# Optimization experiments

Measured on AMD Instinct MI355X. Metric: run time of the kernel, lower is better.

The kernel has to match this reference:

```python
import jax, jax.numpy as jnp
import numpy as np

B, N, D, H = 2, 2048, 1024, 16
DH = D // H
SCALE = DH ** -0.5


def setup_inputs() -> dict:
    key = jax.random.key(0)
    ks = jax.random.split(key, 12)
    s = 0.02
    q = jax.random.normal(ks[0], (B, N, D), jnp.float32)
    k = jax.random.normal(ks[1], (B, N, D), jnp.float32)
    v = jax.random.normal(ks[2], (B, N, D), jnp.float32)
    attn_mask = jax.random.randint(ks[3], (B, 1, N, N), 0, 2).astype(bool)
    Wq = jax.random.normal(ks[4], (D, D), jnp.float32) * s
    bq = jnp.zeros((D,), jnp.float32)
    Wk = jax.random.normal(ks[5], (D, D), jnp.float32) * s
    bk = jnp.zeros((D,), jnp.float32)
    Wv = jax.random.normal(ks[6], (D, D), jnp.float32) * s
    bv = jnp.zeros((D,), jnp.float32)
    Wp = jax.random.normal(ks[7], (D, D), jnp.float32) * s
    bp = jnp.zeros((D,), jnp.float32)
    return {"q": q, "k": k, "v": v, "attn_mask": attn_mask,
            "Wq": Wq, "bq": bq, "Wk": Wk, "bk": bk,
            "Wv": Wv, "bv": bv, "Wp": Wp, "bp": bp}


def _heads(x, W, b):
    # (B, N, D) -> (B, H, N, DH)
    Bx, Nx, _ = x.shape
    return (x @ W + b).reshape(Bx, Nx, H, DH).transpose(0, 2, 1, 3)


def reference(q, k, v, attn_mask, Wq, bq, Wk, bk, Wv, bv, Wp, bp):
    qh = _heads(q, Wq, bq)                 # (B, H, Nq, DH)
    kh = _heads(k, Wk, bk)                 # (B, H, Nk, DH)
    vh = _heads(v, Wv, bv)                 # (B, H, Nk, DH)
    attn_raw = jnp.einsum('bhqd,bhkd->bhqk', qh, kh) * SCALE
    attn = jnp.where(attn_mask, -jnp.inf, attn_raw)   # masked_fill(attn_mask, -inf)
    attn = jax.nn.softmax(attn, axis=-1)
    x = jnp.einsum('bhqk,bhkd->bhqd', attn, vh)       # (B, H, Nq, DH)
    x = x.transpose(0, 2, 1, 3).reshape(q.shape[0], q.shape[1], D)
    return x @ Wp + bp
```

## Files before the change

kernel.cpp:

```cpp
#include <hip/hip_runtime.h>
#include <stdint.h>

typedef short bf16x8 __attribute__((ext_vector_type(8)));
typedef float f32x4 __attribute__((ext_vector_type(4)));

#define DEV __device__ __forceinline__

static constexpr int BB = 2, NN = 2048, DD = 1024, HH = 16, DH = 64;
static constexpr float SCLOG2E = 0.18033688011112042f;

static constexpr size_t OFF_PACK   = 1024;
static constexpr size_t PACK_BYTES = (size_t)BB * NN * (NN / 64) * 8ull;
static constexpr size_t OFF_WT     = OFF_PACK + PACK_BYTES;
static constexpr size_t WT_ONE     = (size_t)DD * DD;
static constexpr size_t HEAD_BYTES = (size_t)BB * HH * NN * DH * 2ull;
static constexpr size_t OFF_QH     = OFF_WT + 4 * WT_ONE * 2;
static constexpr size_t OFF_KH     = OFF_QH + HEAD_BYTES;
static constexpr size_t OFF_VT     = OFF_KH + HEAD_BYTES;
static constexpr size_t OFF_X      = OFF_VT + HEAD_BYTES;
static constexpr size_t OFF_KB     = OFF_X + HEAD_BYTES;
static constexpr size_t OFF_VB     = OFF_KB + HEAD_BYTES;
static constexpr size_t NEED_BIG   = OFF_VB + HEAD_BYTES;

DEV unsigned short f2b(float f) {
  unsigned int u = __builtin_bit_cast(unsigned int, f);
  u = (u + 0x7fffu + ((u >> 16) & 1u)) >> 16;
  return (unsigned short)u;
}

#define GLOAD16(gp, lp) __builtin_amdgcn_global_load_lds(                     \
    (const __attribute__((address_space(1))) void*)(gp),                      \
    (__attribute__((address_space(3))) void*)(lp), 16, 0, 0)

__global__ __launch_bounds__(256) void prep(
    const float* W0, const float* W1, const float* W2, const float* W3,
    unsigned short* wt,
    const float* q, const float* k, const float* v,
    unsigned short* qb, unsigned short* kb, unsigned short* vb, int doCvt,
    const void* msrc, unsigned long long* packed) {
  __shared__ unsigned short T[64][72];
  const int id = blockIdx.x, t = threadIdx.x;

  if (id < 1024) {
    int z = id >> 8, local = id & 255;
    int n0 = (local & 15) * 64, k0 = (local >> 4) * 64;
    const float* W = (z == 0) ? W0 : (z == 1) ? W1 : (z == 2) ? W2 : W3;
    unsigned short* dst = wt + (size_t)z * WT_ONE;
    #pragma unroll
    for (int i = 0; i < 4; i++) {
      int row = i * 16 + (t >> 4), col = 4 * (t & 15);
      float4 vv = *(const float4*)&W[(size_t)(k0 + row) * DD + n0 + col];
      T[row][col + 0] = f2b(vv.x); T[row][col + 1] = f2b(vv.y);
      T[row][col + 2] = f2b(vv.z); T[row][col + 3] = f2b(vv.w);
    }
    __syncthreads();
    #pragma unroll
    for (int i = 0; i < 4; i++) {
      int n = i * 16 + (t >> 4), kk = 4 * (t & 15);
      ushort4 o = make_ushort4(T[kk][n], T[kk + 1][n], T[kk + 2][n], T[kk + 3][n]);
      *(ushort4*)&dst[(size_t)(n0 + n) * DD + k0 + kk] = o;
    }
  } else if (id < 7168) {
    if (!doCvt) return;
    int local = id - 1024;
    int z = local / 2048, bx = local % 2048;
    const float* s = (z == 0) ? q : (z == 1) ? k : v;
    unsigned short* d = (z == 0) ? qb : (z == 1) ? kb : vb;
    size_t i = ((size_t)bx * 256 + t) * 8;
    float4 a = *(const float4*)&s[i];
    float4 b2 = *(const float4*)&s[i + 4];
    unsigned short o[8] = {f2b(a.x),  f2b(a.y),  f2b(a.z),  f2b(a.w),
                           f2b(b2.x), f2b(b2.y), f2b(b2.z), f2b(b2.w)};
    *(uint4*)&d[i] = *(const uint4*)o;
  } else {
    unsigned f = 0;
    const unsigned* m32 = (const unsigned*)msrc;
    #pragma unroll
    for (int i = 0; i < 16; i++) {
      unsigned xv = m32[i];
      if (xv != 0u && xv != 1u) f |= 1u;
      if (xv != 0u && xv != 0x3f800000u) f |= 2u;
    }
    int w = (id - 7168) * 256 + t;
    size_t base = (size_t)(w >> 5) * 2048 + (size_t)(w & 31) * 64;
    unsigned long long bits = 0ull;
    if (!(f & 1u)) {
      const int4* p = (const int4*)msrc + (base >> 2);
      #pragma unroll
      for (int c = 0; c < 16; c++) {
        int4 qv = p[c];
        if (qv.x) bits |= 1ull << (4 * c + 0);
        if (qv.y) bits |= 1ull << (4 * c + 1);
        if (qv.z) bits |= 1ull << (4 * c + 2);
        if (qv.w) bits |= 1ull << (4 * c + 3);
      }
    } else if (!(f & 2u)) {
      const float4* p = (const float4*)msrc + (base >> 2);
      #pragma unroll
      for (int c = 0; c < 16; c++) {
        float4 qv = p[c];
        if (qv.x != 0.f) bits |= 1ull << (4 * c + 0);
        if (qv.y != 0.f) bits |= 1ull << (4 * c + 1);
        if (qv.z != 0.f) bits |= 1ull << (4 * c + 2);
        if (qv.w != 0.f) bits |= 1ull << (4 * c + 3);
      }
    } else {
      const uint4* p = (const uint4*)((const char*)msrc + base);
      #pragma unroll
      for (int c = 0; c < 4; c++) {
        uint4 qv = p[c];
        unsigned vals[4] = {qv.x, qv.y, qv.z, qv.w};
        #pragma unroll
        for (int i = 0; i < 4; i++)
          #pragma unroll
          for (int j = 0; j < 4; j++)
            if ((vals[i] >> (8 * j)) & 0xffu) bits |= 1ull << (16 * c + 4 * i + j);
      }
    }
    packed[w] = bits;
  }
}

template <int PROJ>
__global__ __launch_bounds__(256) void gemm_pl(
    const unsigned short* A0, const unsigned short* A1,
    const unsigned short* A2, const unsigned short* Wt,
    const float* b0, const float* b1, const float* b2, const float* b3,
    unsigned short* dQ, unsigned short* dK, unsigned short* dVt, float* out) {
  __shared__ unsigned short Al[2][128 * 32];
  __shared__ unsigned short Bl[2][128 * 32];
  const int t = threadIdx.x;
  const int w = t >> 6, l = t & 63, lr = l & 15, lg = l >> 4;
  const int wm = (w >> 1) * 64, wn = (w & 1) * 64;

  const int wg = blockIdx.x;
  const int chunk = wg & 7, local = wg >> 3;
  const int colBlk = local >> 2, rowBlk = chunk * 4 + (local & 3);
  const int m0 = rowBlk * 128, n0 = colBlk * 128;
  const int z = PROJ ? 3 : (n0 >> 10);
  const int n0z = PROJ ? n0 : (n0 & 1023);
  const unsigned short* Asrc = PROJ ? A0 : (z == 0 ? A0 : (z == 1 ? A1 : A2));
  const unsigned short* Bsrc = Wt + (size_t)z * WT_ONE;
  const float* bias = PROJ ? b3 : (z == 0 ? b0 : (z == 1 ? b1 : b2));

  const unsigned short* aP =
      Asrc + (size_t)(m0 + w * 32 + (l >> 2)) * DD + (l & 3) * 8;
  const unsigned short* bP =
      Bsrc + (size_t)(n0z + w * 32 + (l >> 2)) * DD + (l & 3) * 8;

  f32x4 acc[4][4];
  #pragma unroll
  for (int i = 0; i < 4; i++)
    #pragma unroll
    for (int j = 0; j < 4; j++) acc[i][j] = (f32x4){0.f, 0.f, 0.f, 0.f};

  auto STAGE = [&](int k0, int buf) {
    GLOAD16(aP + k0,           &Al[buf][(w * 32) * 32]);
    GLOAD16(aP + k0 + 16 * DD, &Al[buf][(w * 32 + 16) * 32]);
    GLOAD16(bP + k0,           &Bl[buf][(w * 32) * 32]);
    GLOAD16(bP + k0 + 16 * DD, &Bl[buf][(w * 32 + 16) * 32]);
  };

  STAGE(0, 0);
  for (int it = 0; it < DD / 32; ++it) {
    if (it + 1 < DD / 32) {
      STAGE((it + 1) * 32, (it + 1) & 1);
      asm volatile("s_waitcnt vmcnt(4)" ::: "memory");
    } else {
      asm volatile("s_waitcnt vmcnt(0)" ::: "memory");
    }
    __builtin_amdgcn_s_barrier();

    const int buf = it & 1;
    bf16x8 af[4], bfr[4];
    #pragma unroll
    for (int mi = 0; mi < 4; mi++)
      af[mi] = *(const bf16x8*)&Al[buf][(wm + mi * 16 + lr) * 32 + lg * 8];
    #pragma unroll
    for (int ni = 0; ni < 4; ni++)
      bfr[ni] = *(const bf16x8*)&Bl[buf][(wn + ni * 16 + lr) * 32 + lg * 8];
    #pragma unroll
    for (int mi = 0; mi < 4; mi++)
      #pragma unroll
      for (int ni = 0; ni < 4; ni++)
        acc[mi][ni] = __builtin_amdgcn_mfma_f32_16x16x32_bf16(
            af[mi], bfr[ni], acc[mi][ni], 0, 0, 0);
    __builtin_amdgcn_s_barrier();
  }

  const float scl = (!PROJ && z == 0) ? SCLOG2E : 1.0f;
  #pragma unroll
  for (int mi = 0; mi < 4; mi++) {
    #pragma unroll
    for (int ni = 0; ni < 4; ni++) {
      int col = n0z + wn + ni * 16 + lr;
      float bv = bias[col];
      int h = col >> 6, dh = col & 63;
      int mbase = m0 + wm + mi * 16 + lg * 4;
      if (PROJ) {
        #pragma unroll
        for (int r = 0; r < 4; r++)
          out[(size_t)(mbase + r) * DD + col] = acc[mi][ni][r] + bv;
      } else if (z == 2) {
        int bq = mbase >> 11, n = mbase & 2047;
        unsigned short o4[4];
        #pragma unroll
        for (int r = 0; r < 4; r++) o4[r] = f2b(acc[mi][ni][r] + bv);
        *(ushort4*)&dVt[(((size_t)(bq * HH + h)) * DH + dh) * NN + n] =
            *(const ushort4*)o4;
      } else {
        unsigned short* dst = (z == 0) ? dQ : dK;
        #pragma unroll
        for (int r = 0; r < 4; r++) {
          int m = mbase + r;
          int bq = m >> 11, n = m & 2047;
          dst[(((size_t)(bq * HH + h)) * NN + n) * DH + dh] =
              f2b((acc[mi][ni][r] + bv) * scl);
        }
      }
    }
  }
}

__global__ __launch_bounds__(256) void gemm_qkv_f32(
    const float* A0, const float* A1, const float* A2,
    const unsigned short* Wt,
    const float* b0, const float* b1, const float* b2,
    unsigned short* dQ, unsigned short* dK, unsigned short* dVt) {
  __shared__ unsigned short Al[128 * 32];
  __shared__ unsigned short Bl[128 * 32];
  const int t = threadIdx.x, z = blockIdx.z;
  const int m0 = blockIdx.y * 128, n0 = blockIdx.x * 128;
  const unsigned short* Bsrc = Wt + (size_t)z * WT_ONE;
  const float* Af = (z == 0) ? A0 : (z == 1) ? A1 : A2;
  const float* bias = (z == 0) ? b0 : (z == 1) ? b1 : b2;
  const int w = t >> 6, l = t & 63, lr = l & 15, lg = l >> 4;
  const int wm = (w >> 1) * 64, wn = (w & 1) * 64;

  f32x4 acc[4][4];
  #pragma unroll
  for (int i = 0; i < 4; i++)
    #pragma unroll
    for (int j = 0; j < 4; j++) acc[i][j] = (f32x4){0.f, 0.f, 0.f, 0.f};

  for (int k0 = 0; k0 < DD; k0 += 32) {
    __syncthreads();
    #pragma unroll
    for (int i = 0; i < 4; i++) {
      int row = i * 32 + (t >> 3), kk = 4 * (t & 7);
      float4 vv = *(const float4*)&Af[(size_t)(m0 + row) * DD + k0 + kk];
      ushort4 o4 = make_ushort4(f2b(vv.x), f2b(vv.y), f2b(vv.z), f2b(vv.w));
      *(ushort4*)&Al[row * 32 + kk] = o4;
    }
    #pragma unroll
    for (int c = 0; c < 2; c++)
      GLOAD16(&Bsrc[(size_t)(n0 + w * 32 + c * 16 + (l >> 2)) * DD + k0 + (l & 3) * 8],
              &Bl[(w * 32 + c * 16) * 32]);
    __syncthreads();

    bf16x8 af[4], bfr[4];
    #pragma unroll
    for (int mi = 0; mi < 4; mi++)
      af[mi] = *(const bf16x8*)&Al[(wm + mi * 16 + lr) * 32 + lg * 8];
    #pragma unroll
    for (int ni = 0; ni < 4; ni++)
      bfr[ni] = *(const bf16x8*)&Bl[(wn + ni * 16 + lr) * 32 + lg * 8];
    #pragma unroll
    for (int mi = 0; mi < 4; mi++)
      #pragma unroll
      for (int ni = 0; ni < 4; ni++)
        acc[mi][ni] = __builtin_amdgcn_mfma_f32_16x16x32_bf16(
            af[mi], bfr[ni], acc[mi][ni], 0, 0, 0);
  }

  const float scl = (z == 0) ? SCLOG2E : 1.0f;
  #pragma unroll
  for (int mi = 0; mi < 4; mi++) {
    #pragma unroll
    for (int ni = 0; ni < 4; ni++) {
      int col = n0 + wn + ni * 16 + lr;
      float bv = bias[col];
      int h = col >> 6, dh = col & 63;
      int mbase = m0 + wm + mi * 16 + lg * 4;
      if (z == 2) {
        int bq = mbase >> 11, n = mbase & 2047;
        unsigned short o4[4];
        #pragma unroll
        for (int r = 0; r < 4; r++) o4[r] = f2b(acc[mi][ni][r] + bv);
        *(ushort4*)&dVt[(((size_t)(bq * HH + h)) * DH + dh) * NN + n] =
            *(const ushort4*)o4;
      } else {
        unsigned short* dst = (z == 0) ? dQ : dK;
        #pragma unroll
        for (int r = 0; r < 4; r++) {
          int m = mbase + r;
          int bq = m >> 11, n = m & 2047;
          dst[(((size_t)(bq * HH + h)) * NN + n) * DH + dh] =
              f2b((acc[mi][ni][r] + bv) * scl);
        }
      }
    }
  }
}

__global__ __launch_bounds__(256) void attn_k(
    const unsigned short* qh, const unsigned short* kh,
    const unsigned short* vht, const unsigned long long* packed,
    unsigned short* x) {
  __shared__ __align__(16) unsigned short Kl[64 * 64];
  __shared__ __align__(16) unsigned short Vl[64 * 64];
  __shared__ __align__(16) unsigned short Pl[4][16 * 64];
  char* KlB = (char*)Kl;
  char* VlB = (char*)Vl;
  const int t = threadIdx.x, w = t >> 6, l = t & 63;
  const int lr = l & 15, lg = l >> 4;
  char* PlB = (char*)&Pl[w][0];

  const int id = blockIdx.x;
  const int xcd = id & 7, j = id >> 3;
  const int bhg = xcd * 4 + (j >> 5);
  const int q0 = (j & 31) * 64;
  const int b = bhg >> 4, h = bhg & 15;
  const size_t bh = (size_t)b * HH + h;
  const unsigned short* Q = qh + bh * (size_t)NN * DH;
  const unsigned short* K = kh + bh * (size_t)NN * DH;
  const unsigned short* V = vht + bh * (size_t)NN * DH;
  const int qrow = q0 + w * 16 + lr;
  const unsigned long long* pmrow =
      packed + ((size_t)b * NN + qrow) * (NN / 64);

  bf16x8 qf[2];
  #pragma unroll
  for (int kc = 0; kc < 2; kc++)
    qf[kc] = *(const bf16x8*)&Q[(size_t)qrow * DH + kc * 32 + lg * 8];

  f32x4 o[4];
  #pragma unroll
  for (int f = 0; f < 4; f++) o[f] = (f32x4){0.f, 0.f, 0.f, 0.f};
  float lsum = 0.f;

  const int srow = t >> 2, sc0 = (t & 3) * 32;
  const int swr = (srow & 7) << 4;
  const int swl = (lr & 7) << 4;
  const int sA = srow * 128 + (sc0 ^ swr);
  const int sB = srow * 128 + ((sc0 + 16) ^ swr);

  const unsigned short* kpp = &K[(size_t)srow * DH + sc0 / 2];
  const unsigned short* vpp = &V[(size_t)srow * NN + sc0 / 2];
  uint4 k0r = *(const uint4*)kpp, k1r = *(const uint4*)(kpp + 8);
  uint4 v0r = *(const uint4*)vpp, v1r = *(const uint4*)(vpp + 8);

  for (int kt = 0; kt < NN / 64; kt++) {
    __syncthreads();
    *(uint4*)&KlB[sA] = k0r;
    *(uint4*)&KlB[sB] = k1r;
    *(uint4*)&VlB[sA] = v0r;
    *(uint4*)&VlB[sB] = v1r;
    __syncthreads();
    if (kt + 1 < NN / 64) {
      kpp += 64 * DH;
      vpp += 64;
      k0r = *(const uint4*)kpp;  k1r = *(const uint4*)(kpp + 8);
      v0r = *(const uint4*)vpp;  v1r = *(const uint4*)(vpp + 8);
    }

    unsigned long long mw = pmrow[kt];

    f32x4 sv4[4];
    __builtin_amdgcn_s_setprio(1);
    #pragma unroll
    for (int f = 0; f < 4; f++) {
      f32x4 s = (f32x4){0.f, 0.f, 0.f, 0.f};
      bf16x8 kf0 = *(const bf16x8*)&KlB[(16 * f + lr) * 128 + ((lg * 16) ^ swl)];
      bf16x8 kf1 = *(const bf16x8*)&KlB[(16 * f + lr) * 128 + ((64 + lg * 16) ^ swl)];
      s = __builtin_amdgcn_mfma_f32_16x16x32_bf16(kf0, qf[0], s, 0, 0, 0);
      s = __builtin_amdgcn_mfma_f32_16x16x32_bf16(kf1, qf[1], s, 0, 0, 0);
      sv4[f] = s;
    }
    __builtin_amdgcn_s_setprio(0);

    float part = 0.f;
    #pragma unroll
    for (int f = 0; f < 4; f++) {
      unsigned nib = (unsigned)(mw >> (16 * f + 4 * lg)) & 0xFu;
      float pv[4];
      #pragma unroll
      for (int r = 0; r < 4; r++) {
        float s = ((nib >> r) & 1u) ? -30000.f : sv4[f][r];
        pv[r] = __builtin_amdgcn_exp2f(s);
        part += pv[r];
      }
      unsigned w0, w1;
      asm("v_cvt_pk_bf16_f32 %0, %1, %2" : "=v"(w0) : "v"(pv[0]), "v"(pv[1]));
      asm("v_cvt_pk_bf16_f32 %0, %1, %2" : "=v"(w1) : "v"(pv[2]), "v"(pv[3]));
      *(uint2*)&PlB[lr * 128 + ((f * 32 + lg * 8) ^ swl)] = make_uint2(w0, w1);
    }
    lsum += part;
    asm volatile("s_waitcnt lgkmcnt(0)" ::: "memory");
    __builtin_amdgcn_sched_barrier(0);

    bf16x8 pf0 = *(const bf16x8*)&PlB[lr * 128 + ((lg * 16) ^ swl)];
    bf16x8 pf1 = *(const bf16x8*)&PlB[lr * 128 + ((64 + lg * 16) ^ swl)];
    __builtin_amdgcn_s_setprio(1);
    #pragma unroll
    for (int f = 0; f < 4; f++) {
      bf16x8 vf0 = *(const bf16x8*)&VlB[(16 * f + lr) * 128 + ((lg * 16) ^ swl)];
      o[f] = __builtin_amdgcn_mfma_f32_16x16x32_bf16(vf0, pf0, o[f], 0, 0, 0);
      bf16x8 vf1 = *(const bf16x8*)&VlB[(16 * f + lr) * 128 + ((64 + lg * 16) ^ swl)];
      o[f] = __builtin_amdgcn_mfma_f32_16x16x32_bf16(vf1, pf1, o[f], 0, 0, 0);
    }
    __builtin_amdgcn_s_setprio(0);
  }

  lsum += __shfl_xor(lsum, 16);
  lsum += __shfl_xor(lsum, 32);
  float inv = 1.f / fmaxf(lsum, 1e-30f);
  #pragma unroll
  for (int f = 0; f < 4; f++) {
    unsigned w0, w1;
    float a0 = o[f][0] * inv, a1 = o[f][1] * inv;
    float a2 = o[f][2] * inv, a3 = o[f][3] * inv;
    asm("v_cvt_pk_bf16_f32 %0, %1, %2" : "=v"(w0) : "v"(a0), "v"(a1));
    asm("v_cvt_pk_bf16_f32 %0, %1, %2" : "=v"(w1) : "v"(a2), "v"(a3));
    *(uint2*)&x[((size_t)b * NN + qrow) * DD + h * DH + 16 * f + lg * 4] =
        make_uint2(w0, w1);
  }
}

extern "C" void kernel_launch(void* const* d_in, const int* in_sizes, int n_in,
                              void* d_out, int out_size, void* d_ws, size_t ws_size,
                              hipStream_t stream) {
  const float* q  = (const float*)d_in[0];
  const float* k  = (const float*)d_in[1];
  const float* v  = (const float*)d_in[2];
  const void*  mk = d_in[3];
  const float* Wq = (const float*)d_in[4];
  const float* bq = (const float*)d_in[5];
  const float* Wk = (const float*)d_in[6];
  const float* bk = (const float*)d_in[7];
  const float* Wv = (const float*)d_in[8];
  const float* bv = (const float*)d_in[9];
  const float* Wp = (const float*)d_in[10];
  const float* bp = (const float*)d_in[11];
  float* out = (float*)d_out;
  char* ws = (char*)d_ws;

  unsigned long long* packed = (unsigned long long*)(ws + OFF_PACK);
  unsigned short* wt  = (unsigned short*)(ws + OFF_WT);
  unsigned short* qhp = (unsigned short*)(ws + OFF_QH);
  unsigned short* khp = (unsigned short*)(ws + OFF_KH);
  unsigned short* vht = (unsigned short*)(ws + OFF_VT);
  unsigned short* x   = (unsigned short*)(ws + OFF_X);
  unsigned short* qb  = (unsigned short*)(ws + OFF_X);
  unsigned short* kb  = (unsigned short*)(ws + OFF_KB);
  unsigned short* vb  = (unsigned short*)(ws + OFF_VB);

  const bool big = ws_size >= NEED_BIG;

  prep<<<dim3(7680), 256, 0, stream>>>(Wq, Wk, Wv, Wp, wt, q, k, v,
                                       qb, kb, vb, big ? 1 : 0, mk, packed);
  if (big) {
    gemm_pl<0><<<dim3(768), 256, 0, stream>>>(qb, kb, vb, wt,
                                              bq, bk, bv, bp,
                                              qhp, khp, vht, nullptr);
  } else {
    gemm_qkv_f32<<<dim3(8, 32, 3), 256, 0, stream>>>(q, k, v, wt, bq, bk, bv,
                                                     qhp, khp, vht);
  }
  attn_k<<<dim3(1024), 256, 0, stream>>>(qhp, khp, vht, packed, x);
  gemm_pl<1><<<dim3(256), 256, 0, stream>>>(x, nullptr, nullptr, wt,
                                            bq, bk, bv, bp,
                                            nullptr, nullptr, nullptr, out);
}
```

Before: 163.0 us.

## Triple-buffer GEMM LDS stages and double attention KV tile to 128

The projection GEMM moves from two LDS buffers to three and prefetches two k-steps ahead, with vmcnt waits adjusted so more global-load latency is hidden. The attention kernel now stages 128 keys per sync instead of 64 and processes them as two 64-wide sub-tiles, which halves the barrier count and makes each thread issue larger register prefetches. In exchange, LDS use and register pressure rise in both kernels, which may lower occupancy.

```diff
diff --git a/kernel.cpp b/kernel.cpp
--- a/kernel.cpp
+++ b/kernel.cpp
@@ -127,8 +127,8 @@
     const unsigned short* A2, const unsigned short* Wt,
     const float* b0, const float* b1, const float* b2, const float* b3,
     unsigned short* dQ, unsigned short* dK, unsigned short* dVt, float* out) {
-  __shared__ unsigned short Al[2][128 * 32];
-  __shared__ unsigned short Bl[2][128 * 32];
+  __shared__ unsigned short Al[3][128 * 32];
+  __shared__ unsigned short Bl[3][128 * 32];
   const int t = threadIdx.x;
   const int w = t >> 6, l = t & 63, lr = l & 15, lg = l >> 4;
   const int wm = (w >> 1) * 64, wn = (w & 1) * 64;
@@ -162,23 +162,26 @@
   };
 
   STAGE(0, 0);
+  STAGE(32, 1);
+  int bcur = 0, bnext = 2;
   for (int it = 0; it < DD / 32; ++it) {
-    if (it + 1 < DD / 32) {
-      STAGE((it + 1) * 32, (it + 1) & 1);
+    if (it + 2 < DD / 32) {
+      STAGE((it + 2) * 32, bnext);
+      asm volatile("s_waitcnt vmcnt(8)" ::: "memory");
+    } else if (it + 2 == DD / 32) {
       asm volatile("s_waitcnt vmcnt(4)" ::: "memory");
     } else {
       asm volatile("s_waitcnt vmcnt(0)" ::: "memory");
     }
     __builtin_amdgcn_s_barrier();
 
-    const int buf = it & 1;
     bf16x8 af[4], bfr[4];
     #pragma unroll
     for (int mi = 0; mi < 4; mi++)
-      af[mi] = *(const bf16x8*)&Al[buf][(wm + mi * 16 + lr) * 32 + lg * 8];
+      af[mi] = *(const bf16x8*)&Al[bcur][(wm + mi * 16 + lr) * 32 + lg * 8];
     #pragma unroll
     for (int ni = 0; ni < 4; ni++)
-      bfr[ni] = *(const bf16x8*)&Bl[buf][(wn + ni * 16 + lr) * 32 + lg * 8];
+      bfr[ni] = *(const bf16x8*)&Bl[bcur][(wn + ni * 16 + lr) * 32 + lg * 8];
     #pragma unroll
     for (int mi = 0; mi < 4; mi++)
       #pragma unroll
@@ -186,6 +189,8 @@
         acc[mi][ni] = __builtin_amdgcn_mfma_f32_16x16x32_bf16(
             af[mi], bfr[ni], acc[mi][ni], 0, 0, 0);
     __builtin_amdgcn_s_barrier();
+    bcur = (bcur == 2) ? 0 : bcur + 1;
+    bnext = (bnext == 2) ? 0 : bnext + 1;
   }
 
   const float scl = (!PROJ && z == 0) ? SCLOG2E : 1.0f;
@@ -307,8 +312,8 @@
     const unsigned short* qh, const unsigned short* kh,
     const unsigned short* vht, const unsigned long long* packed,
     unsigned short* x) {
-  __shared__ __align__(16) unsigned short Kl[64 * 64];
-  __shared__ __align__(16) unsigned short Vl[64 * 64];
+  __shared__ __align__(16) unsigned short Kl[128 * 64];
+  __shared__ __align__(16) unsigned short Vl[64 * 128];
   __shared__ __align__(16) unsigned short Pl[4][16 * 64];
   char* KlB = (char*)Kl;
   char* VlB = (char*)Vl;
@@ -339,77 +344,99 @@
   for (int f = 0; f < 4; f++) o[f] = (f32x4){0.f, 0.f, 0.f, 0.f};
   float lsum = 0.f;
 
-  const int srow = t >> 2, sc0 = (t & 3) * 32;
-  const int swr = (srow & 7) << 4;
+  const int srowK = t >> 1;
+  const int swrK = (srowK & 7) << 4;
+  const int srowV = t >> 2;
+  const int swrV = (srowV & 7) << 4;
   const int swl = (lr & 7) << 4;
-  const int sA = srow * 128 + (sc0 ^ swr);
-  const int sB = srow * 128 + ((sc0 + 16) ^ swr);
-
-  const unsigned short* kpp = &K[(size_t)srow * DH + sc0 / 2];
-  const unsigned short* vpp = &V[(size_t)srow * NN + sc0 / 2];
-  uint4 k0r = *(const uint4*)kpp, k1r = *(const uint4*)(kpp + 8);
-  uint4 v0r = *(const uint4*)vpp, v1r = *(const uint4*)(vpp + 8);
-
-  for (int kt = 0; kt < NN / 64; kt++) {
+  int sKa[4], sVa[4];
+  #pragma unroll
+  for (int jj = 0; jj < 4; jj++) {
+    int cK = (t & 1) * 64 + jj * 16;
+    sKa[jj] = srowK * 128 + (cK ^ swrK);
+    int cV = (t & 3) * 64 + jj * 16;
+    sVa[jj] = srowV * 256 + (cV & 128) + ((cV & 127) ^ swrV);
+  }
+  const unsigned short* kp = &K[(size_t)srowK * DH + (t & 1) * 32];
+  const unsigned short* vp = &V[(size_t)srowV * NN + (t & 3) * 32];
+  uint4 kr[4], vr[4];
+  #pragma unroll
+  for (int jj = 0; jj < 4; jj++) {
+    kr[jj] = *(const uint4*)(kp + jj * 8);
+    vr[jj] = *(const uint4*)(vp + jj * 8);
+  }
+
+  for (int kt = 0; kt < NN / 128; kt++) {
     __syncthreads();
-    *(uint4*)&KlB[sA] = k0r;
-    *(uint4*)&KlB[sB] = k1r;
-    *(uint4*)&VlB[sA] = v0r;
-    *(uint4*)&VlB[sB] = v1r;
+    #pragma unroll
+    for (int jj = 0; jj < 4; jj++) {
+      *(uint4*)&KlB[sKa[jj]] = kr[jj];
+      *(uint4*)&VlB[sVa[jj]] = vr[jj];
+    }
     __syncthreads();
-    if (kt + 1 < NN / 64) {
-      kpp += 64 * DH;
-      vpp += 64;
-      k0r = *(const uint4*)kpp;  k1r = *(const uint4*)(kpp + 8);
-      v0r = *(const uint4*)vpp;  v1r = *(const uint4*)(vpp + 8);
-    }
-
-    unsigned long long mw = pmrow[kt];
-
-    f32x4 sv4[4];
-    __builtin_amdgcn_s_setprio(1);
-    #pragma unroll
-    for (int f = 0; f < 4; f++) {
-      f32x4 s = (f32x4){0.f, 0.f, 0.f, 0.f};
-      bf16x8 kf0 = *(const bf16x8*)&KlB[(16 * f + lr) * 128 + ((lg * 16) ^ swl)];
-      bf16x8 kf1 = *(const bf16x8*)&KlB[(16 * f + lr) * 128 + ((64 + lg * 16) ^ swl)];
-      s = __builtin_amdgcn_mfma_f32_16x16x32_bf16(kf0, qf[0], s, 0, 0, 0);
-      s = __builtin_amdgcn_mfma_f32_16x16x32_bf16(kf1, qf[1], s, 0, 0, 0);
-      sv4[f] = s;
-    }
-    __builtin_amdgcn_s_setprio(0);
-
-    float part = 0.f;
-    #pragma unroll
-    for (int f = 0; f < 4; f++) {
-      unsigned nib = (unsigned)(mw >> (16 * f + 4 * lg)) & 0xFu;
-      float pv[4];
-      #pragma unroll
-      for (int r = 0; r < 4; r++) {
-        float s = ((nib >> r) & 1u) ? -30000.f : sv4[f][r];
-        pv[r] = __builtin_amdgcn_exp2f(s);
-        part += pv[r];
-      }
-      unsigned w0, w1;
-      asm("v_cvt_pk_bf16_f32 %0, %1, %2" : "=v"(w0) : "v"(pv[0]), "v"(pv[1]));
-      asm("v_cvt_pk_bf16_f32 %0, %1, %2" : "=v"(w1) : "v"(pv[2]), "v"(pv[3]));
-      *(uint2*)&PlB[lr * 128 + ((f * 32 + lg * 8) ^ swl)] = make_uint2(w0, w1);
-    }
-    lsum += part;
-    asm volatile("s_waitcnt lgkmcnt(0)" ::: "memory");
-    __builtin_amdgcn_sched_barrier(0);
-
-    bf16x8 pf0 = *(const bf16x8*)&PlB[lr * 128 + ((lg * 16) ^ swl)];
-    bf16x8 pf1 = *(const bf16x8*)&PlB[lr * 128 + ((64 + lg * 16) ^ swl)];
-    __builtin_amdgcn_s_setprio(1);
-    #pragma unroll
-    for (int f = 0; f < 4; f++) {
-      bf16x8 vf0 = *(const bf16x8*)&VlB[(16 * f + lr) * 128 + ((lg * 16) ^ swl)];
-      o[f] = __builtin_amdgcn_mfma_f32_16x16x32_bf16(vf0, pf0, o[f], 0, 0, 0);
-      bf16x8 vf1 = *(const bf16x8*)&VlB[(16 * f + lr) * 128 + ((64 + lg * 16) ^ swl)];
-      o[f] = __builtin_amdgcn_mfma_f32_16x16x32_bf16(vf1, pf1, o[f], 0, 0, 0);
-    }
-    __builtin_amdgcn_s_setprio(0);
+    if (kt + 1 < NN / 128) {
+      kp += 128 * DH;
+      vp += 128;
+      #pragma unroll
+      for (int jj = 0; jj < 4; jj++) {
+        kr[jj] = *(const uint4*)(kp + jj * 8);
+        vr[jj] = *(const uint4*)(vp + jj * 8);
+      }
+    }
+    unsigned long long mw0 = pmrow[2 * kt];
+    unsigned long long mw1 = pmrow[2 * kt + 1];
+
+    #pragma unroll
+    for (int s = 0; s < 2; s++) {
+      unsigned long long mw = s ? mw1 : mw0;
+
+      f32x4 sv4[4];
+      __builtin_amdgcn_s_setprio(1);
+      #pragma unroll
+      for (int f = 0; f < 4; f++) {
+        f32x4 sx = (f32x4){0.f, 0.f, 0.f, 0.f};
+        const int rb = (s * 64 + 16 * f + lr) * 128;
+        bf16x8 kf0 = *(const bf16x8*)&KlB[rb + ((lg * 16) ^ swl)];
+        bf16x8 kf1 = *(const bf16x8*)&KlB[rb + ((64 + lg * 16) ^ swl)];
+        sx = __builtin_amdgcn_mfma_f32_16x16x32_bf16(kf0, qf[0], sx, 0, 0, 0);
+        sx = __builtin_amdgcn_mfma_f32_16x16x32_bf16(kf1, qf[1], sx, 0, 0, 0);
+        sv4[f] = sx;
+      }
+      __builtin_amdgcn_s_setprio(0);
+
+      float part = 0.f;
+      #pragma unroll
+      for (int f = 0; f < 4; f++) {
+        unsigned nib = (unsigned)(mw >> (16 * f + 4 * lg)) & 0xFu;
+        float pv[4];
+        #pragma unroll
+        for (int r = 0; r < 4; r++) {
+          float sc = ((nib >> r) & 1u) ? -30000.f : sv4[f][r];
+          pv[r] = __builtin_amdgcn_exp2f(sc);
+          part += pv[r];
+        }
+        unsigned w0, w1;
+        asm("v_cvt_pk_bf16_f32 %0, %1, %2" : "=v"(w0) : "v"(pv[0]), "v"(pv[1]));
+        asm("v_cvt_pk_bf16_f32 %0, %1, %2" : "=v"(w1) : "v"(pv[2]), "v"(pv[3]));
+        *(uint2*)&PlB[lr * 128 + ((f * 32 + lg * 8) ^ swl)] = make_uint2(w0, w1);
+      }
+      lsum += part;
+      asm volatile("s_waitcnt lgkmcnt(0)" ::: "memory");
+      __builtin_amdgcn_sched_barrier(0);
+
+      bf16x8 pf0 = *(const bf16x8*)&PlB[lr * 128 + ((lg * 16) ^ swl)];
+      bf16x8 pf1 = *(const bf16x8*)&PlB[lr * 128 + ((64 + lg * 16) ^ swl)];
+      __builtin_amdgcn_s_setprio(1);
+      #pragma unroll
+      for (int f = 0; f < 4; f++) {
+        const int rb = (16 * f + lr) * 256 + s * 128;
+        bf16x8 vf0 = *(const bf16x8*)&VlB[rb + ((lg * 16) ^ swl)];
+        o[f] = __builtin_amdgcn_mfma_f32_16x16x32_bf16(vf0, pf0, o[f], 0, 0, 0);
+        bf16x8 vf1 = *(const bf16x8*)&VlB[rb + ((64 + lg * 16) ^ swl)];
+        o[f] = __builtin_amdgcn_mfma_f32_16x16x32_bf16(vf1, pf1, o[f], 0, 0, 0);
+      }
+      __builtin_amdgcn_s_setprio(0);
+    }
   }
 
   lsum += __shfl_xor(lsum, 16);
```

New measurement: 264.4 us. 62.2% more time.

## Process 128-key tiles per barrier pair in attention kernel and prefetch mask words

Applied to the files above, without the earlier changes.

The attention kernel now stages 128 keys of K and V into LDS per iteration and runs two 64-key sub-steps between each pair of barriers, halving the number of __syncthreads and loop iterations. Mask words for the next tile are also prefetched alongside the K/V register prefetch, so the mask load is no longer issued on the critical path. The cost is doubled LDS for K/V and more prefetch registers, which may lower occupancy.

```diff
diff --git a/kernel.cpp b/kernel.cpp
--- a/kernel.cpp
+++ b/kernel.cpp
@@ -307,8 +307,8 @@
     const unsigned short* qh, const unsigned short* kh,
     const unsigned short* vht, const unsigned long long* packed,
     unsigned short* x) {
-  __shared__ __align__(16) unsigned short Kl[64 * 64];
-  __shared__ __align__(16) unsigned short Vl[64 * 64];
+  __shared__ __align__(16) unsigned short Kl[128 * 64];
+  __shared__ __align__(16) unsigned short Vl[64 * 128];
   __shared__ __align__(16) unsigned short Pl[4][16 * 64];
   char* KlB = (char*)Kl;
   char* VlB = (char*)Vl;
@@ -339,43 +339,42 @@
   for (int f = 0; f < 4; f++) o[f] = (f32x4){0.f, 0.f, 0.f, 0.f};
   float lsum = 0.f;
 
-  const int srow = t >> 2, sc0 = (t & 3) * 32;
-  const int swr = (srow & 7) << 4;
+  const int srowK = t >> 1, halfK = t & 1;
+  const int swrK = (srowK & 7) << 4;
+  const int sK0 = srowK * 128 + ((halfK * 64 +  0) ^ swrK);
+  const int sK1 = srowK * 128 + ((halfK * 64 + 16) ^ swrK);
+  const int sK2 = srowK * 128 + ((halfK * 64 + 32) ^ swrK);
+  const int sK3 = srowK * 128 + ((halfK * 64 + 48) ^ swrK);
+  const int srowV = t >> 2, qrtV = t & 3;
+  const int swrV = (srowV & 7) << 4;
+  const int cV0 = qrtV * 64 +  0, cV1 = qrtV * 64 + 16;
+  const int cV2 = qrtV * 64 + 32, cV3 = qrtV * 64 + 48;
+  const int sV0 = srowV * 256 + (cV0 & 128) + ((cV0 & 127) ^ swrV);
+  const int sV1 = srowV * 256 + (cV1 & 128) + ((cV1 & 127) ^ swrV);
+  const int sV2 = srowV * 256 + (cV2 & 128) + ((cV2 & 127) ^ swrV);
+  const int sV3 = srowV * 256 + (cV3 & 128) + ((cV3 & 127) ^ swrV);
   const int swl = (lr & 7) << 4;
-  const int sA = srow * 128 + (sc0 ^ swr);
-  const int sB = srow * 128 + ((sc0 + 16) ^ swr);
-
-  const unsigned short* kpp = &K[(size_t)srow * DH + sc0 / 2];
-  const unsigned short* vpp = &V[(size_t)srow * NN + sc0 / 2];
-  uint4 k0r = *(const uint4*)kpp, k1r = *(const uint4*)(kpp + 8);
-  uint4 v0r = *(const uint4*)vpp, v1r = *(const uint4*)(vpp + 8);
-
-  for (int kt = 0; kt < NN / 64; kt++) {
-    __syncthreads();
-    *(uint4*)&KlB[sA] = k0r;
-    *(uint4*)&KlB[sB] = k1r;
-    *(uint4*)&VlB[sA] = v0r;
-    *(uint4*)&VlB[sB] = v1r;
-    __syncthreads();
-    if (kt + 1 < NN / 64) {
-      kpp += 64 * DH;
-      vpp += 64;
-      k0r = *(const uint4*)kpp;  k1r = *(const uint4*)(kpp + 8);
-      v0r = *(const uint4*)vpp;  v1r = *(const uint4*)(vpp + 8);
-    }
-
-    unsigned long long mw = pmrow[kt];
-
+
+  const unsigned short* kpp = &K[(size_t)srowK * DH + halfK * 32];
+  const unsigned short* vpp = &V[(size_t)srowV * NN + qrtV * 32];
+  uint4 kr0 = *(const uint4*)(kpp +  0), kr1 = *(const uint4*)(kpp +  8);
+  uint4 kr2 = *(const uint4*)(kpp + 16), kr3 = *(const uint4*)(kpp + 24);
+  uint4 vr0 = *(const uint4*)(vpp +  0), vr1 = *(const uint4*)(vpp +  8);
+  uint4 vr2 = *(const uint4*)(vpp + 16), vr3 = *(const uint4*)(vpp + 24);
+  unsigned long long mwa = pmrow[0], mwb = pmrow[1];
+
+  auto sub = [&](int s, unsigned long long mw) {
     f32x4 sv4[4];
     __builtin_amdgcn_s_setprio(1);
     #pragma unroll
     for (int f = 0; f < 4; f++) {
-      f32x4 s = (f32x4){0.f, 0.f, 0.f, 0.f};
-      bf16x8 kf0 = *(const bf16x8*)&KlB[(16 * f + lr) * 128 + ((lg * 16) ^ swl)];
-      bf16x8 kf1 = *(const bf16x8*)&KlB[(16 * f + lr) * 128 + ((64 + lg * 16) ^ swl)];
-      s = __builtin_amdgcn_mfma_f32_16x16x32_bf16(kf0, qf[0], s, 0, 0, 0);
-      s = __builtin_amdgcn_mfma_f32_16x16x32_bf16(kf1, qf[1], s, 0, 0, 0);
-      sv4[f] = s;
+      f32x4 sx = (f32x4){0.f, 0.f, 0.f, 0.f};
+      const int rb = (s * 64 + 16 * f + lr) * 128;
+      bf16x8 kf0 = *(const bf16x8*)&KlB[rb + ((lg * 16) ^ swl)];
+      bf16x8 kf1 = *(const bf16x8*)&KlB[rb + ((64 + lg * 16) ^ swl)];
+      sx = __builtin_amdgcn_mfma_f32_16x16x32_bf16(kf0, qf[0], sx, 0, 0, 0);
+      sx = __builtin_amdgcn_mfma_f32_16x16x32_bf16(kf1, qf[1], sx, 0, 0, 0);
+      sv4[f] = sx;
     }
     __builtin_amdgcn_s_setprio(0);
 
@@ -386,8 +385,8 @@
       float pv[4];
       #pragma unroll
       for (int r = 0; r < 4; r++) {
-        float s = ((nib >> r) & 1u) ? -30000.f : sv4[f][r];
-        pv[r] = __builtin_amdgcn_exp2f(s);
+        float sc = ((nib >> r) & 1u) ? -30000.f : sv4[f][r];
+        pv[r] = __builtin_amdgcn_exp2f(sc);
         part += pv[r];
       }
       unsigned w0, w1;
@@ -404,12 +403,43 @@
     __builtin_amdgcn_s_setprio(1);
     #pragma unroll
     for (int f = 0; f < 4; f++) {
-      bf16x8 vf0 = *(const bf16x8*)&VlB[(16 * f + lr) * 128 + ((lg * 16) ^ swl)];
+      const int rb = (16 * f + lr) * 256 + s * 128;
+      bf16x8 vf0 = *(const bf16x8*)&VlB[rb + ((lg * 16) ^ swl)];
       o[f] = __builtin_amdgcn_mfma_f32_16x16x32_bf16(vf0, pf0, o[f], 0, 0, 0);
-      bf16x8 vf1 = *(const bf16x8*)&VlB[(16 * f + lr) * 128 + ((64 + lg * 16) ^ swl)];
+      bf16x8 vf1 = *(const bf16x8*)&VlB[rb + ((64 + lg * 16) ^ swl)];
       o[f] = __builtin_amdgcn_mfma_f32_16x16x32_bf16(vf1, pf1, o[f], 0, 0, 0);
     }
     __builtin_amdgcn_s_setprio(0);
+  };
+
+  for (int kt = 0; kt < NN / 128; kt++) {
+    __syncthreads();
+    *(uint4*)&KlB[sK0] = kr0;
+    *(uint4*)&KlB[sK1] = kr1;
+    *(uint4*)&KlB[sK2] = kr2;
+    *(uint4*)&KlB[sK3] = kr3;
+    *(uint4*)&VlB[sV0] = vr0;
+    *(uint4*)&VlB[sV1] = vr1;
+    *(uint4*)&VlB[sV2] = vr2;
+    *(uint4*)&VlB[sV3] = vr3;
+    __syncthreads();
+    unsigned long long mwaN = mwa, mwbN = mwb;
+    if (kt + 1 < NN / 128) {
+      kpp += 128 * DH;
+      vpp += 128;
+      kr0 = *(const uint4*)(kpp +  0); kr1 = *(const uint4*)(kpp +  8);
+      kr2 = *(const uint4*)(kpp + 16); kr3 = *(const uint4*)(kpp + 24);
+      vr0 = *(const uint4*)(vpp +  0); vr1 = *(const uint4*)(vpp +  8);
+      vr2 = *(const uint4*)(vpp + 16); vr3 = *(const uint4*)(vpp + 24);
+      mwaN = pmrow[2 * kt + 2];
+      mwbN = pmrow[2 * kt + 3];
+    }
+
+    sub(0, mwa);
+    sub(1, mwb);
+
+    mwa = mwaN;
+    mwb = mwbN;
   }
 
   lsum += __shfl_xor(lsum, 16);
```

After: 175.2 us. 7.4% more time.
